# Optimization experiments

Hardware: AMD Instinct MI355X
Metric: run time of the kernel (lower is better)

Reference implementation:

```python
import jax, jax.numpy as jnp
import numpy as np

N_USERS = 50000
N_ENTITIES = 100000
N_FACTORS = 8
N_RELATIONS = 17  # weight has n_relations-1 = 16 rows
EMB = 64
N_EDGES = 2_000_000
NNZ = 2_000_000
SLOPE = 0.2


def setup_inputs() -> dict:
    key = jax.random.key(0)
    ks = jax.random.split(key, 16)
    inp = {
        "entity_emb": jax.random.normal(ks[0], (N_ENTITIES, EMB), jnp.float32),
        "user_emb": jax.random.normal(ks[1], (N_USERS, EMB), jnp.float32),
        "latent_emb": jax.random.normal(ks[2], (N_FACTORS, EMB), jnp.float32),
        "edge_index": jax.random.randint(ks[3], (2, N_EDGES), 0, N_ENTITIES, jnp.int32),
        "edge_type": jax.random.randint(ks[4], (N_EDGES,), 1, N_RELATIONS, jnp.int32),
        "interact_rows": jax.random.randint(ks[5], (NNZ,), 0, N_USERS, jnp.int32),
        "interact_cols": jax.random.randint(ks[6], (NNZ,), 0, N_ENTITIES, jnp.int32),
        "interact_vals": jax.random.uniform(ks[7], (NNZ,), jnp.float32),
        "weight": jax.random.normal(ks[8], (N_RELATIONS - 1, EMB), jnp.float32),
        "entity_cate_set": jax.random.randint(ks[9], (N_ENTITIES,), 1, 33, jnp.int32),
        # params (torch Linear convention: y = x @ W.T + b)
        "W_user_att": jax.random.normal(ks[10], (N_FACTORS, N_FACTORS), jnp.float32) * 0.1,
        "b_user_att": jnp.zeros((N_FACTORS,), jnp.float32),
        "W_weight_att": jax.random.normal(ks[11], (N_RELATIONS - 1, N_RELATIONS - 1), jnp.float32) * 0.1,
        "b_weight_att": jnp.zeros((N_RELATIONS - 1,), jnp.float32),
        "W1": jax.random.normal(ks[12], (EMB, EMB), jnp.float32) * 0.1,
        "b1": jnp.zeros((EMB,), jnp.float32),
        "W2": jax.random.normal(ks[13], (EMB, EMB), jnp.float32) * 0.1,
        "b2": jnp.zeros((EMB,), jnp.float32),
    }
    return inp


def _lin(x, W, b):
    return x @ W.T + b


def reference(entity_emb, user_emb, latent_emb, edge_index, edge_type,
              interact_rows, interact_cols, interact_vals, weight, entity_cate_set,
              W_user_att, b_user_att, W_weight_att, b_weight_att, W1, b1, W2, b2):
    head, tail = edge_index[0], edge_index[1]

    # KG aggregate: gather-multiply-scatter_mean (is_div=False branch)
    neigh = entity_emb[tail] * weight[edge_type - 1]            # [E, C]
    sums = jax.ops.segment_sum(neigh, head, num_segments=N_ENTITIES)
    cnt = jax.ops.segment_sum(jnp.ones((neigh.shape[0],), neigh.dtype),
                              head, num_segments=N_ENTITIES)
    entity_agg = sums / jnp.maximum(cnt, 1.0)[:, None]          # [N_ent, C]

    # user aggregate: sparse mm (COO) interact_mat @ entity_emb
    user_agg = jax.ops.segment_sum(interact_vals[:, None] * entity_emb[interact_cols],
                                   interact_rows, num_segments=N_USERS)  # [U, C]

    # user -> latent interest attention
    score_ = _lin(user_emb, W1, b1) @ _lin(latent_emb, W1, b1).T          # [U, F]
    score = jax.nn.softmax(jax.nn.leaky_relu(_lin(score_, W_user_att, b_user_att), SLOPE), axis=1)  # [U, F]

    score_rp = _lin(latent_emb, W2, b2) @ _lin(weight, W2, b2).T          # [F, R-1]
    latent_new = jax.nn.softmax(jax.nn.leaky_relu(_lin(score_rp, W_weight_att, b_weight_att), SLOPE), axis=-1) @ weight  # [F, C]

    # (disen_weight * score).sum(dim=1) == score @ latent_new
    user_agg = user_agg * (score @ latent_new) + user_agg
    return (entity_agg, user_agg, latent_new)
```

## Files before the change

### kernel.cpp

```cpp
#include <hip/hip_runtime.h>
#include <hip/hip_bf16.h>

#define N_USERS    50000
#define N_ENTITIES 100000
#define EMB        64
#define N_EDGES    2000000
#define NNZ        2000000
#define SLOPE      0.2f

#define KROWS   256
#define KSHIFT  8
#define NBK     391
#define UROWS   128
#define USHIFT  7
#define NBU     391
#define CAPK    8192
#define CAPU    7680
#define CHUNK   8192
#define PB      ((N_EDGES + CHUNK - 1) / CHUNK)

__global__ __launch_bounds__(512) void hist_both(const int* __restrict__ head,
                                                 const int* __restrict__ urows,
                                                 int* __restrict__ kgOffs,
                                                 int* __restrict__ uOffs) {
    __shared__ int lhk[NBK];
    __shared__ int lhu[NBU];
    int tid = threadIdx.x;
    for (int t = tid; t < NBK; t += 512) lhk[t] = 0;
    for (int t = tid; t < NBU; t += 512) lhu[t] = 0;
    __syncthreads();
    int base = blockIdx.x * CHUNK;
#pragma unroll 4
    for (int j = 0; j < CHUNK / 512; ++j) {
        int i = base + j * 512 + tid;
        if (i < N_EDGES) atomicAdd(&lhk[head[i] >> KSHIFT], 1);
        if (i < NNZ)     atomicAdd(&lhu[urows[i] >> USHIFT], 1);
    }
    __syncthreads();
    for (int t = tid; t < NBK; t += 512) { int c = lhk[t]; if (c) atomicAdd(&kgOffs[t], c); }
    for (int t = tid; t < NBU; t += 512) { int c = lhu[t]; if (c) atomicAdd(&uOffs[t], c); }
}

__global__ __launch_bounds__(512) void scan_both(int* __restrict__ kgOffs,
                                                 int* __restrict__ kgCur,
                                                 int* __restrict__ uOffs,
                                                 int* __restrict__ uCur) {
    __shared__ int tsum[512];
    int n     = (blockIdx.x == 0) ? NBK : NBU;
    int* offs = (blockIdx.x == 0) ? kgOffs : uOffs;
    int* cur  = (blockIdx.x == 0) ? kgCur  : uCur;
    int tid = threadIdx.x;
    int v = (tid < n) ? offs[tid] : 0;
    tsum[tid] = v;
    __syncthreads();
    for (int off = 1; off < 512; off <<= 1) {
        int t = (tid >= off) ? tsum[tid - off] : 0;
        __syncthreads();
        tsum[tid] += t;
        __syncthreads();
    }
    if (tid < n) { int e = tsum[tid] - v; offs[tid] = e; cur[tid] = e; }
    if (tid == n - 1) offs[n] = tsum[tid];
}

__global__ __launch_bounds__(512) void scatter_both(const int* __restrict__ head,
                                                    const int* __restrict__ tail,
                                                    const int* __restrict__ etype,
                                                    int* __restrict__ kgCur,
                                                    int* __restrict__ kgPay,
                                                    const int* __restrict__ urows,
                                                    const int* __restrict__ ucols,
                                                    const float* __restrict__ uvals,
                                                    int* __restrict__ uCur,
                                                    int2* __restrict__ uPay) {
    __shared__ int lh[NBK];
    __shared__ int lb[NBK];
    int tid = threadIdx.x;
    bool isKg = blockIdx.x < PB;
    int base = (isKg ? blockIdx.x : blockIdx.x - PB) * CHUNK;

    for (int t = tid; t < NBK; t += 512) lh[t] = 0;
    __syncthreads();
    if (isKg) {
#pragma unroll 4
        for (int j = 0; j < CHUNK / 512; ++j) {
            int i = base + j * 512 + tid;
            if (i < N_EDGES) atomicAdd(&lh[head[i] >> KSHIFT], 1);
        }
    } else {
#pragma unroll 4
        for (int j = 0; j < CHUNK / 512; ++j) {
            int i = base + j * 512 + tid;
            if (i < NNZ) atomicAdd(&lh[urows[i] >> USHIFT], 1);
        }
    }
    __syncthreads();
    int* cur = isKg ? kgCur : uCur;
    for (int t = tid; t < NBK; t += 512) {
        int c = lh[t];
        lb[t] = c ? atomicAdd(&cur[t], c) : 0;
        lh[t] = 0;
    }
    __syncthreads();
    if (isKg) {
#pragma unroll 4
        for (int j = 0; j < CHUNK / 512; ++j) {
            int i = base + j * 512 + tid;
            if (i < N_EDGES) {
                int h = head[i];
                int b = h >> KSHIFT;
                int p = lb[b] + atomicAdd(&lh[b], 1);
                kgPay[p] = tail[i] | ((etype[i] - 1) << 17) | ((h & (KROWS - 1)) << 21);
            }
        }
    } else {
#pragma unroll 4
        for (int j = 0; j < CHUNK / 512; ++j) {
            int i = base + j * 512 + tid;
            if (i < NNZ) {
                int r = urows[i];
                int b = r >> USHIFT;
                int p = lb[b] + atomicAdd(&lh[b], 1);
                uPay[p] = make_int2(ucols[i] | ((r & (UROWS - 1)) << 17),
                                    __float_as_int(uvals[i]));
            }
        }
    }
}

__global__ __launch_bounds__(1024, 8) void acc_both(
        const int* __restrict__ kgPay, const int* __restrict__ kgOffs,
        const int2* __restrict__ uPay, const int* __restrict__ uOffs,
        const float* __restrict__ entity_emb,
        const float* __restrict__ weight,
        const float* __restrict__ user_emb,
        const float* __restrict__ P,
        const float* __restrict__ cvec,
        const float* __restrict__ W_user_att,
        const float* __restrict__ b_user_att,
        const float* __restrict__ latent_new,
        float* __restrict__ ent_out,
        float* __restrict__ user_out) {
    __shared__ long long smem8[7873];
    int t = threadIdx.x, d = t & 63, wv = t >> 6;

    if (blockIdx.x < NBK) {
        int* spay = (int*)smem8;
        int* lcnt = spay + CAPK;
        int* lofs = lcnt + KROWS;
        int* sc   = lofs + KROWS + 1;
        int start = kgOffs[blockIdx.x], end = kgOffs[blockIdx.x + 1];
        int n = end - start; if (n > CAPK) n = CAPK;

        if (t < KROWS) lcnt[t] = 0;
        __syncthreads();
        for (int i = t; i < n; i += 1024)
            atomicAdd(&lcnt[(kgPay[start + i] >> 21) & (KROWS - 1)], 1);
        __syncthreads();
        if (t < KROWS) sc[t] = lcnt[t];
        __syncthreads();
        for (int off = 1; off < KROWS; off <<= 1) {
            int v = (t < KROWS && t >= off) ? sc[t - off] : 0;
            __syncthreads();
            if (t < KROWS) sc[t] += v;
            __syncthreads();
        }
        if (t < KROWS) { int e = sc[t] - lcnt[t]; lofs[t] = e; lcnt[t] = e; }
        if (t == 0) lofs[KROWS] = n;
        __syncthreads();
        for (int i = t; i < n; i += 1024) {
            int v = kgPay[start + i];
            int p = atomicAdd(&lcnt[(v >> 21) & (KROWS - 1)], 1);
            spay[p] = v;
        }
        __syncthreads();

        int rowbase = blockIdx.x * KROWS;
        for (int rr = 0; rr < KROWS / 16; ++rr) {
            int r = wv * (KROWS / 16) + rr;
            int gr = rowbase + r;
            if (gr >= N_ENTITIES) break;
            int s0 = lofs[r], e0 = lofs[r + 1];
            int cnt = e0 - s0;
            float acc = 0.f;
            int i = s0;
            for (; i + 7 < e0; i += 8) {
                float a0 = 0.f, a1 = 0.f;
#pragma unroll
                for (int u = 0; u < 8; u += 2) {
                    int va = spay[i + u], vb = spay[i + u + 1];
                    a0 += entity_emb[(va & 0x1FFFF) * EMB + d] * weight[((va >> 17) & 15) * EMB + d];
                    a1 += entity_emb[(vb & 0x1FFFF) * EMB + d] * weight[((vb >> 17) & 15) * EMB + d];
                }
                acc += a0 + a1;
            }
            for (; i < e0; ++i) {
                int v = spay[i];
                acc += entity_emb[(v & 0x1FFFF) * EMB + d] * weight[((v >> 17) & 15) * EMB + d];
            }
            for (int j = start + CAPK; j < end; ++j) {
                int v = kgPay[j];
                if (((v >> 21) & (KROWS - 1)) == r) {
                    acc += entity_emb[(v & 0x1FFFF) * EMB + d] * weight[((v >> 17) & 15) * EMB + d];
                    ++cnt;
                }
            }
            ent_out[gr * EMB + d] = acc / fmaxf((float)cnt, 1.f);
        }
    } else {
        int2* spay = (int2*)smem8;
        int* lcnt = (int*)(spay + CAPU);
        int* lofs = lcnt + UROWS;
        int* sc   = lofs + UROWS + 1;
        int bk = blockIdx.x - NBK;
        int start = uOffs[bk], end = uOffs[bk + 1];
        int n = end - start; if (n > CAPU) n = CAPU;

        if (t < UROWS) lcnt[t] = 0;
        __syncthreads();
        for (int i = t; i < n; i += 1024)
            atomicAdd(&lcnt[(uPay[start + i].x >> 17) & (UROWS - 1)], 1);
        __syncthreads();
        if (t < UROWS) sc[t] = lcnt[t];
        __syncthreads();
        for (int off = 1; off < UROWS; off <<= 1) {
            int v = (t < UROWS && t >= off) ? sc[t - off] : 0;
            __syncthreads();
            if (t < UROWS) sc[t] += v;
            __syncthreads();
        }
        if (t < UROWS) { int e = sc[t] - lcnt[t]; lofs[t] = e; lcnt[t] = e; }
        if (t == 0) lofs[UROWS] = n;
        __syncthreads();
        for (int i = t; i < n; i += 1024) {
            int2 v = uPay[start + i];
            int p = atomicAdd(&lcnt[(v.x >> 17) & (UROWS - 1)], 1);
            spay[p] = v;
        }
        __syncthreads();

        int rowbase = bk * UROWS;
        for (int rr = 0; rr < UROWS / 16; ++rr) {
            int r = wv * (UROWS / 16) + rr;
            int gr = rowbase + r;
            if (gr >= N_USERS) break;
            int s0 = lofs[r], e0 = lofs[r + 1];
            float acc = 0.f;
            int i = s0;
            for (; i + 7 < e0; i += 8) {
                float a0 = 0.f, a1 = 0.f;
#pragma unroll
                for (int u = 0; u < 8; u += 2) {
                    int2 va = spay[i + u], vb = spay[i + u + 1];
                    a0 += __int_as_float(va.y) * entity_emb[(va.x & 0x1FFFF) * EMB + d];
                    a1 += __int_as_float(vb.y) * entity_emb[(vb.x & 0x1FFFF) * EMB + d];
                }
                acc += a0 + a1;
            }
            for (; i < e0; ++i) {
                int2 v = spay[i];
                acc += __int_as_float(v.y) * entity_emb[(v.x & 0x1FFFF) * EMB + d];
            }
            for (int j = start + CAPU; j < end; ++j) {
                int2 v = uPay[j];
                if (((v.x >> 17) & (UROWS - 1)) == r)
                    acc += __int_as_float(v.y) * entity_emb[(v.x & 0x1FFFF) * EMB + d];
            }

            float ue = user_emb[gr * EMB + d];
            float s[8];
#pragma unroll
            for (int f = 0; f < 8; ++f) s[f] = ue * P[d * 8 + f];
#pragma unroll
            for (int off = 32; off; off >>= 1) {
#pragma unroll
                for (int f = 0; f < 8; ++f) s[f] += __shfl_xor(s[f], off, 64);
            }
#pragma unroll
            for (int f = 0; f < 8; ++f) s[f] += cvec[f];
            float att[8];
            float mx = -1e30f;
#pragma unroll
            for (int k = 0; k < 8; ++k) {
                float a = b_user_att[k];
#pragma unroll
                for (int j = 0; j < 8; ++j) a += s[j] * W_user_att[k * 8 + j];
                a = a > 0.f ? a : SLOPE * a;
                att[k] = a;
                mx = fmaxf(mx, a);
            }
            float sum = 0.f;
#pragma unroll
            for (int k = 0; k < 8; ++k) { att[k] = __expf(att[k] - mx); sum += att[k]; }
            float inv = 1.f / sum;
            float g = 0.f;
#pragma unroll
            for (int f = 0; f < 8; ++f) g += att[f] * inv * latent_new[f * EMB + d];
            user_out[gr * EMB + d] = acc * (1.f + g);
        }
    }
}

__global__ void small_dense(const float* __restrict__ latent_emb,
                            const float* __restrict__ weight,
                            const float* __restrict__ W_weight_att,
                            const float* __restrict__ b_weight_att,
                            const float* __restrict__ W1,
                            const float* __restrict__ b1,
                            const float* __restrict__ W2,
                            const float* __restrict__ b2,
                            float* __restrict__ P_out,
                            float* __restrict__ c_out,
                            float* __restrict__ latent_new_out) {
    __shared__ float lat1[8 * 64];
    __shared__ float lat2[8 * 64];
    __shared__ float wl2[16 * 64];
    __shared__ float srp[8 * 16];
    __shared__ float soft[8 * 16];
    int l = threadIdx.x;

    for (int f = 0; f < 8; ++f) {
        float a1 = b1[l], a2 = b2[l];
        for (int k = 0; k < 64; ++k) {
            float le = latent_emb[f * 64 + k];
            a1 += le * W1[l * 64 + k];
            a2 += le * W2[l * 64 + k];
        }
        lat1[f * 64 + l] = a1;
        lat2[f * 64 + l] = a2;
    }
    for (int r = 0; r < 16; ++r) {
        float a = b2[l];
        for (int k = 0; k < 64; ++k) a += weight[r * 64 + k] * W2[l * 64 + k];
        wl2[r * 64 + l] = a;
    }
    __syncthreads();

    for (int f = 0; f < 8; ++f) {
        float p = 0.f;
        for (int d = 0; d < 64; ++d) p += W1[d * 64 + l] * lat1[f * 64 + d];
        P_out[l * 8 + f] = p;
    }
    if (l < 8) {
        float cc = 0.f;
        for (int d = 0; d < 64; ++d) cc += b1[d] * lat1[l * 64 + d];
        c_out[l] = cc;
    }
    for (int idx = l; idx < 128; idx += 64) {
        int f = idx >> 4, r = idx & 15;
        float a = 0.f;
        for (int d = 0; d < 64; ++d) a += lat2[f * 64 + d] * wl2[r * 64 + d];
        srp[idx] = a;
    }
    __syncthreads();

    if (l < 8) {
        int f = l;
        float att[16];
        float mx = -1e30f;
        for (int k = 0; k < 16; ++k) {
            float a = b_weight_att[k];
            for (int j = 0; j < 16; ++j) a += srp[f * 16 + j] * W_weight_att[k * 16 + j];
            a = a > 0.f ? a : SLOPE * a;
            att[k] = a;
            mx = fmaxf(mx, a);
        }
        float s = 0.f;
        for (int k = 0; k < 16; ++k) { att[k] = expf(att[k] - mx); s += att[k]; }
        float inv = 1.f / s;
        for (int k = 0; k < 16; ++k) soft[f * 16 + k] = att[k] * inv;
    }
    __syncthreads();

    for (int f = 0; f < 8; ++f) {
        float a = 0.f;
        for (int r = 0; r < 16; ++r) a += soft[f * 16 + r] * weight[r * 64 + l];
        latent_new_out[f * 64 + l] = a;
    }
}

__global__ void kg_scatter(const int* __restrict__ head, const int* __restrict__ tail,
                           const int* __restrict__ etype,
                           const float* __restrict__ entity_emb,
                           const float* __restrict__ weight,
                           float* __restrict__ sums, float* __restrict__ cnt) {
    int gid = blockIdx.x * blockDim.x + threadIdx.x;
    int e = gid >> 6, d = threadIdx.x & 63;
    if (e >= N_EDGES) return;
    int h = head[e], t = tail[e], w = etype[e] - 1;
    float v = entity_emb[t * EMB + d] * weight[w * EMB + d];
    unsafeAtomicAdd(&sums[h * EMB + d], v);
    if (d == 0) unsafeAtomicAdd(&cnt[h], 1.0f);
}

__global__ void user_scatter(const int* __restrict__ rows, const int* __restrict__ cols,
                             const float* __restrict__ vals,
                             const float* __restrict__ entity_emb,
                             float* __restrict__ user_sums) {
    int gid = blockIdx.x * blockDim.x + threadIdx.x;
    int e = gid >> 6, d = threadIdx.x & 63;
    if (e >= NNZ) return;
    float v = vals[e] * entity_emb[cols[e] * EMB + d];
    unsafeAtomicAdd(&user_sums[rows[e] * EMB + d], v);
}

__global__ void entity_div(float* __restrict__ ent, const float* __restrict__ cnt) {
    int gid = blockIdx.x * blockDim.x + threadIdx.x;
    if (gid >= N_ENTITIES * EMB) return;
    float c = cnt[gid >> 6];
    ent[gid] = ent[gid] / fmaxf(c, 1.0f);
}

__global__ void user_finalize(const float* __restrict__ user_emb,
                              const float* __restrict__ P,
                              const float* __restrict__ c,
                              const float* __restrict__ W_user_att,
                              const float* __restrict__ b_user_att,
                              const float* __restrict__ latent_new,
                              float* __restrict__ user_out) {
    int gid = blockIdx.x * blockDim.x + threadIdx.x;
    int u = gid >> 6, lane = threadIdx.x & 63;
    if (u >= N_USERS) return;
    float ue = user_emb[u * 64 + lane];
    float s[8];
#pragma unroll
    for (int f = 0; f < 8; ++f) s[f] = ue * P[lane * 8 + f];
#pragma unroll
    for (int off = 32; off; off >>= 1)
#pragma unroll
        for (int f = 0; f < 8; ++f) s[f] += __shfl_xor(s[f], off, 64);
#pragma unroll
    for (int f = 0; f < 8; ++f) s[f] += c[f];
    float att[8], mx = -1e30f;
#pragma unroll
    for (int k = 0; k < 8; ++k) {
        float a = b_user_att[k];
#pragma unroll
        for (int j = 0; j < 8; ++j) a += s[j] * W_user_att[k * 8 + j];
        a = a > 0.f ? a : SLOPE * a;
        att[k] = a;
        mx = fmaxf(mx, a);
    }
    float sum = 0.f;
#pragma unroll
    for (int k = 0; k < 8; ++k) { att[k] = expf(att[k] - mx); sum += att[k]; }
    float inv = 1.f / sum, g = 0.f;
#pragma unroll
    for (int f = 0; f < 8; ++f) g += att[f] * inv * latent_new[f * 64 + lane];
    float ua = user_out[u * 64 + lane];
    user_out[u * 64 + lane] = ua * (1.f + g);
}

extern "C" void kernel_launch(void* const* d_in, const int* in_sizes, int n_in,
                              void* d_out, int out_size, void* d_ws, size_t ws_size,
                              hipStream_t stream) {
    const float* entity_emb   = (const float*)d_in[0];
    const float* user_emb     = (const float*)d_in[1];
    const float* latent_emb   = (const float*)d_in[2];
    const int*   edge_index   = (const int*)d_in[3];
    const int*   edge_type    = (const int*)d_in[4];
    const int*   irows        = (const int*)d_in[5];
    const int*   icols        = (const int*)d_in[6];
    const float* ivals        = (const float*)d_in[7];
    const float* weight       = (const float*)d_in[8];
    const float* W_user_att   = (const float*)d_in[10];
    const float* b_user_att   = (const float*)d_in[11];
    const float* W_weight_att = (const float*)d_in[12];
    const float* b_weight_att = (const float*)d_in[13];
    const float* W1           = (const float*)d_in[14];
    const float* b1           = (const float*)d_in[15];
    const float* W2           = (const float*)d_in[16];
    const float* b2           = (const float*)d_in[17];

    float* out      = (float*)d_out;
    float* ent_out  = out;
    float* user_out = out + (size_t)N_ENTITIES * EMB;
    float* lat_out  = user_out + (size_t)N_USERS * EMB;

    const int* head = edge_index;
    const int* tail = edge_index + N_EDGES;

    int* ws_i = (int*)d_ws;
    int*   kgOffs = ws_i;
    int*   uOffs  = kgOffs + (NBK + 1);
    int*   kgCur  = uOffs + (NBU + 1);
    int*   uCur   = kgCur + NBK;
    int*   kgPay  = uCur + NBU;
    int2*  uPay   = (int2*)(kgPay + N_EDGES);
    float* Pbuf   = (float*)(uPay + NNZ);
    float* cbuf   = Pbuf + 64 * 8;
    size_t need_bytes = (size_t)((NBK + 1) + (NBU + 1) + NBK + NBU +
                                 N_EDGES + 2 * (size_t)NNZ + 512 + 8) * 4;

    if (ws_size >= need_bytes) {
        hipMemsetAsync(kgOffs, 0, (size_t)((NBK + 1) + (NBU + 1)) * sizeof(int), stream);

        hist_both<<<PB, 512, 0, stream>>>(head, irows, kgOffs, uOffs);
        scan_both<<<2, 512, 0, stream>>>(kgOffs, kgCur, uOffs, uCur);
        scatter_both<<<2 * PB, 512, 0, stream>>>(head, tail, edge_type, kgCur, kgPay,
                                                 irows, icols, ivals, uCur, uPay);
        small_dense<<<1, 64, 0, stream>>>(latent_emb, weight, W_weight_att,
                                          b_weight_att, W1, b1, W2, b2,
                                          Pbuf, cbuf, lat_out);
        acc_both<<<NBK + NBU, 1024, 0, stream>>>(kgPay, kgOffs, uPay, uOffs,
                                                 entity_emb, weight, user_emb,
                                                 Pbuf, cbuf, W_user_att, b_user_att,
                                                 lat_out, ent_out, user_out);
    } else {
        float* cnt   = (float*)d_ws;
        float* Pbuf2 = cnt + N_ENTITIES;
        float* cbuf2 = Pbuf2 + 64 * 8;
        hipMemsetAsync(ent_out, 0,
                       (size_t)(N_ENTITIES + N_USERS) * EMB * sizeof(float), stream);
        hipMemsetAsync(cnt, 0, N_ENTITIES * sizeof(float), stream);
        int blocks_edges = (N_EDGES * 64) / 256;
        kg_scatter<<<blocks_edges, 256, 0, stream>>>(head, tail, edge_type, entity_emb,
                                                     weight, ent_out, cnt);
        user_scatter<<<blocks_edges, 256, 0, stream>>>(irows, icols, ivals, entity_emb,
                                                       user_out);
        small_dense<<<1, 64, 0, stream>>>(latent_emb, weight, W_weight_att,
                                          b_weight_att, W1, b1, W2, b2,
                                          Pbuf2, cbuf2, lat_out);
        user_finalize<<<(N_USERS * 64) / 256, 256, 0, stream>>>(user_emb, Pbuf2, cbuf2,
                                                                W_user_att, b_user_att,
                                                                lat_out, user_out);
        entity_div<<<(N_ENTITIES * EMB) / 256, 256, 0, stream>>>(ent_out, cnt);
    }
}
```

Before: 442.4 us.

## Use persistent work-queue blocks for accumulation and fold small_dense into scatter

The accumulation kernel now launches a fixed 512 persistent blocks that pull bucket indices from a global atomic counter, taking user buckets first and then KG buckets, instead of one block per bucket. The small dense attention computation moves into an extra block of the scatter kernel, which removes a separate launch. The scatter kernel also keeps the head/row indices it loaded for the histogram in registers and reuses them in the placement pass rather than reloading them. These changes aim to cut launch overhead, tail imbalance and redundant global loads, at the cost of a serialising atomic per work item and higher register pressure in scatter.

```diff
diff --git a/kernel.cpp b/kernel.cpp
--- a/kernel.cpp
+++ b/kernel.cpp
@@ -1,5 +1,4 @@
 #include <hip/hip_runtime.h>
-#include <hip/hip_bf16.h>
 
 #define N_USERS    50000
 #define N_ENTITIES 100000
@@ -17,7 +16,10 @@
 #define CAPK    8192
 #define CAPU    7680
 #define CHUNK   8192
+#define EPT     (CHUNK / 512)
 #define PB      ((N_EDGES + CHUNK - 1) / CHUNK)
+#define NQ      (NBK + NBU)
+#define ACCBLK  512
 
 __global__ __launch_bounds__(512) void hist_both(const int* __restrict__ head,
                                                  const int* __restrict__ urows,
@@ -31,7 +33,7 @@
     __syncthreads();
     int base = blockIdx.x * CHUNK;
 #pragma unroll 4
-    for (int j = 0; j < CHUNK / 512; ++j) {
+    for (int j = 0; j < EPT; ++j) {
         int i = base + j * 512 + tid;
         if (i < N_EDGES) atomicAdd(&lhk[head[i] >> KSHIFT], 1);
         if (i < NNZ)     atomicAdd(&lhu[urows[i] >> USHIFT], 1);
@@ -63,6 +65,105 @@
     if (tid == n - 1) offs[n] = tsum[tid];
 }
 
+__device__ void small_dense_body(int l,
+                                 const float* __restrict__ latent_emb,
+                                 const float* __restrict__ weight,
+                                 const float* __restrict__ W_weight_att,
+                                 const float* __restrict__ b_weight_att,
+                                 const float* __restrict__ W1,
+                                 const float* __restrict__ b1,
+                                 const float* __restrict__ W2,
+                                 const float* __restrict__ b2,
+                                 float* __restrict__ P_out,
+                                 float* __restrict__ c_out,
+                                 float* __restrict__ latent_new_out) {
+    __shared__ float lat1[8 * 64];
+    __shared__ float lat2[8 * 64];
+    __shared__ float wl2[16 * 64];
+    __shared__ float srp[8 * 16];
+    __shared__ float soft[8 * 16];
+
+    if (l < 64) {
+        for (int f = 0; f < 8; ++f) {
+            float a1 = b1[l], a2 = b2[l];
+            for (int k = 0; k < 64; ++k) {
+                float le = latent_emb[f * 64 + k];
+                a1 += le * W1[l * 64 + k];
+                a2 += le * W2[l * 64 + k];
+            }
+            lat1[f * 64 + l] = a1;
+            lat2[f * 64 + l] = a2;
+        }
+        for (int r = 0; r < 16; ++r) {
+            float a = b2[l];
+            for (int k = 0; k < 64; ++k) a += weight[r * 64 + k] * W2[l * 64 + k];
+            wl2[r * 64 + l] = a;
+        }
+    }
+    __syncthreads();
+
+    if (l < 64) {
+        for (int f = 0; f < 8; ++f) {
+            float p = 0.f;
+            for (int d = 0; d < 64; ++d) p += W1[d * 64 + l] * lat1[f * 64 + d];
+            P_out[l * 8 + f] = p;
+        }
+        if (l < 8) {
+            float cc = 0.f;
+            for (int d = 0; d < 64; ++d) cc += b1[d] * lat1[l * 64 + d];
+            c_out[l] = cc;
+        }
+        for (int idx = l; idx < 128; idx += 64) {
+            int f = idx >> 4, r = idx & 15;
+            float a = 0.f;
+            for (int d = 0; d < 64; ++d) a += lat2[f * 64 + d] * wl2[r * 64 + d];
+            srp[idx] = a;
+        }
+    }
+    __syncthreads();
+
+    if (l < 8) {
+        int f = l;
+        float att[16];
+        float mx = -1e30f;
+        for (int k = 0; k < 16; ++k) {
+            float a = b_weight_att[k];
+            for (int j = 0; j < 16; ++j) a += srp[f * 16 + j] * W_weight_att[k * 16 + j];
+            a = a > 0.f ? a : SLOPE * a;
+            att[k] = a;
+            mx = fmaxf(mx, a);
+        }
+        float s = 0.f;
+        for (int k = 0; k < 16; ++k) { att[k] = expf(att[k] - mx); s += att[k]; }
+        float inv = 1.f / s;
+        for (int k = 0; k < 16; ++k) soft[f * 16 + k] = att[k] * inv;
+    }
+    __syncthreads();
+
+    if (l < 64) {
+        for (int f = 0; f < 8; ++f) {
+            float a = 0.f;
+            for (int r = 0; r < 16; ++r) a += soft[f * 16 + r] * weight[r * 64 + l];
+            latent_new_out[f * 64 + l] = a;
+        }
+    }
+}
+
+__global__ void small_dense(const float* __restrict__ latent_emb,
+                            const float* __restrict__ weight,
+                            const float* __restrict__ W_weight_att,
+                            const float* __restrict__ b_weight_att,
+                            const float* __restrict__ W1,
+                            const float* __restrict__ b1,
+                            const float* __restrict__ W2,
+                            const float* __restrict__ b2,
+                            float* __restrict__ P_out,
+                            float* __restrict__ c_out,
+                            float* __restrict__ latent_new_out) {
+    small_dense_body(threadIdx.x, latent_emb, weight, W_weight_att, b_weight_att,
+                     W1, b1, W2, b2, P_out, c_out, latent_new_out);
+}
+
 __global__ __launch_bounds__(512) void scatter_both(const int* __restrict__ head,
                                                     const int* __restrict__ tail,
                                                     const int* __restrict__ etype,
@@ -72,30 +173,46 @@
                                                     const int* __restrict__ ucols,
                                                     const float* __restrict__ uvals,
                                                     int* __restrict__ uCur,
-                                                    int2* __restrict__ uPay) {
+                                                    int2* __restrict__ uPay,
+                                                    const float* __restrict__ latent_emb,
+                                                    const float* __restrict__ weight,
+                                                    const float* __restrict__ W_weight_att,
+                                                    const float* __restrict__ b_weight_att,
+                                                    const float* __restrict__ W1,
+                                                    const float* __restrict__ b1,
+                                                    const float* __restrict__ W2,
+                                                    const float* __restrict__ b2,
+                                                    float* __restrict__ Pbuf,
+                                                    float* __restrict__ cbuf,
+                                                    float* __restrict__ lat_out) {
+    if (blockIdx.x == 2 * PB) {
+        small_dense_body(threadIdx.x, latent_emb, weight, W_weight_att,
+                         b_weight_att, W1, b1, W2, b2, Pbuf, cbuf, lat_out);
+        return;
+    }
+
     __shared__ int lh[NBK];
     __shared__ int lb[NBK];
     int tid = threadIdx.x;
     bool isKg = blockIdx.x < PB;
     int base = (isKg ? blockIdx.x : blockIdx.x - PB) * CHUNK;
+    int nTot = isKg ? N_EDGES : NNZ;
+    int shift = isKg ? KSHIFT : USHIFT;
+    const int* src = isKg ? head : urows;
+    int* cur = isKg ? kgCur : uCur;
 
     for (int t = tid; t < NBK; t += 512) lh[t] = 0;
     __syncthreads();
-    if (isKg) {
-#pragma unroll 4
-        for (int j = 0; j < CHUNK / 512; ++j) {
-            int i = base + j * 512 + tid;
-            if (i < N_EDGES) atomicAdd(&lh[head[i] >> KSHIFT], 1);
-        }
-    } else {
-#pragma unroll 4
-        for (int j = 0; j < CHUNK / 512; ++j) {
-            int i = base + j * 512 + tid;
-            if (i < NNZ) atomicAdd(&lh[urows[i] >> USHIFT], 1);
-        }
-    }
-    __syncthreads();
-    int* cur = isKg ? kgCur : uCur;
+
+    int hreg[EPT];
+#pragma unroll
+    for (int j = 0; j < EPT; ++j) {
+        int i = base + j * 512 + tid;
+        int h = (i < nTot) ? src[i] : -1;
+        hreg[j] = h;
+        if (h >= 0) atomicAdd(&lh[h >> shift], 1);
+    }
+    __syncthreads();
     for (int t = tid; t < NBK; t += 512) {
         int c = lh[t];
         lb[t] = c ? atomicAdd(&cur[t], c) : 0;
@@ -103,25 +220,25 @@
     }
     __syncthreads();
     if (isKg) {
-#pragma unroll 4
-        for (int j = 0; j < CHUNK / 512; ++j) {
-            int i = base + j * 512 + tid;
-            if (i < N_EDGES) {
-                int h = head[i];
+#pragma unroll
+        for (int j = 0; j < EPT; ++j) {
+            int h = hreg[j];
+            if (h >= 0) {
+                int i = base + j * 512 + tid;
                 int b = h >> KSHIFT;
                 int p = lb[b] + atomicAdd(&lh[b], 1);
                 kgPay[p] = tail[i] | ((etype[i] - 1) << 17) | ((h & (KROWS - 1)) << 21);
             }
         }
     } else {
-#pragma unroll 4
-        for (int j = 0; j < CHUNK / 512; ++j) {
-            int i = base + j * 512 + tid;
-            if (i < NNZ) {
-                int r = urows[i];
-                int b = r >> USHIFT;
+#pragma unroll
+        for (int j = 0; j < EPT; ++j) {
+            int h = hreg[j];
+            if (h >= 0) {
+                int i = base + j * 512 + tid;
+                int b = h >> USHIFT;
                 int p = lb[b] + atomicAdd(&lh[b], 1);
-                uPay[p] = make_int2(ucols[i] | ((r & (UROWS - 1)) << 17),
+                uPay[p] = make_int2(ucols[i] | ((h & (UROWS - 1)) << 17),
                                     __float_as_int(uvals[i]));
             }
         }
@@ -139,243 +256,176 @@
         const float* __restrict__ W_user_att,
         const float* __restrict__ b_user_att,
         const float* __restrict__ latent_new,
+        int* __restrict__ qCtr,
         float* __restrict__ ent_out,
         float* __restrict__ user_out) {
     __shared__ long long smem8[7873];
+    __shared__ int sbk;
     int t = threadIdx.x, d = t & 63, wv = t >> 6;
 
-    if (blockIdx.x < NBK) {
-        int* spay = (int*)smem8;
-        int* lcnt = spay + CAPK;
-        int* lofs = lcnt + KROWS;
-        int* sc   = lofs + KROWS + 1;
-        int start = kgOffs[blockIdx.x], end = kgOffs[blockIdx.x + 1];
-        int n = end - start; if (n > CAPK) n = CAPK;
-
-        if (t < KROWS) lcnt[t] = 0;
+    for (;;) {
         __syncthreads();
-        for (int i = t; i < n; i += 1024)
-            atomicAdd(&lcnt[(kgPay[start + i] >> 21) & (KROWS - 1)], 1);
+        if (t == 0) sbk = atomicAdd(qCtr, 1);
         __syncthreads();
-        if (t < KROWS) sc[t] = lcnt[t];
-        __syncthreads();
-        for (int off = 1; off < KROWS; off <<= 1) {
-            int v = (t < KROWS && t >= off) ? sc[t - off] : 0;
-            __syncthreads();
-            if (t < KROWS) sc[t] += v;
-            __syncthreads();
-        }
-        if (t < KROWS) { int e = sc[t] - lcnt[t]; lofs[t] = e; lcnt[t] = e; }
-        if (t == 0) lofs[KROWS] = n;
-        __syncthreads();
-        for (int i = t; i < n; i += 1024) {
-            int v = kgPay[start + i];
-            int p = atomicAdd(&lcnt[(v >> 21) & (KROWS - 1)], 1);
-            spay[p] = v;
-        }
-        __syncthreads();
-
-        int rowbase = blockIdx.x * KROWS;
-        for (int rr = 0; rr < KROWS / 16; ++rr) {
-            int r = wv * (KROWS / 16) + rr;
-            int gr = rowbase + r;
-            if (gr >= N_ENTITIES) break;
-            int s0 = lofs[r], e0 = lofs[r + 1];
-            int cnt = e0 - s0;
-            float acc = 0.f;
-            int i = s0;
-            for (; i + 7 < e0; i += 8) {
-                float a0 = 0.f, a1 = 0.f;
-#pragma unroll
-                for (int u = 0; u < 8; u += 2) {
-                    int va = spay[i + u], vb = spay[i + u + 1];
-                    a0 += entity_emb[(va & 0x1FFFF) * EMB + d] * weight[((va >> 17) & 15) * EMB + d];
-                    a1 += entity_emb[(vb & 0x1FFFF) * EMB + d] * weight[((vb >> 17) & 15) * EMB + d];
-                }
-                acc += a0 + a1;
-            }
-            for (; i < e0; ++i) {
-                int v = spay[i];
-                acc += entity_emb[(v & 0x1FFFF) * EMB + d] * weight[((v >> 17) & 15) * EMB + d];
-            }
-            for (int j = start + CAPK; j < end; ++j) {
-                int v = kgPay[j];
-                if (((v >> 21) & (KROWS - 1)) == r) {
+        int q = sbk;
+        if (q >= NQ) return;
+
+        if (q < NBU) {
+            int2* spay = (int2*)smem8;
+            int* lcnt = (int*)(spay + CAPU);
+            int* lofs = lcnt + UROWS;
+            int* sc   = lofs + UROWS + 1;
+            int bk = q;
+            int start = uOffs[bk], end = uOffs[bk + 1];
+            int n = end - start; if (n > CAPU) n = CAPU;
+
+            if (t < UROWS) lcnt[t] = 0;
+            __syncthreads();
+            for (int i = t; i < n; i += 1024)
+                atomicAdd(&lcnt[(uPay[start + i].x >> 17) & (UROWS - 1)], 1);
+            __syncthreads();
+            if (t < UROWS) sc[t] = lcnt[t];
+            __syncthreads();
+            for (int off = 1; off < UROWS; off <<= 1) {
+                int v = (t < UROWS && t >= off) ? sc[t - off] : 0;
+                __syncthreads();
+                if (t < UROWS) sc[t] += v;
+                __syncthreads();
+            }
+            if (t < UROWS) { int e = sc[t] - lcnt[t]; lofs[t] = e; lcnt[t] = e; }
+            if (t == 0) lofs[UROWS] = n;
+            __syncthreads();
+            for (int i = t; i < n; i += 1024) {
+                int2 v = uPay[start + i];
+                int p = atomicAdd(&lcnt[(v.x >> 17) & (UROWS - 1)], 1);
+                spay[p] = v;
+            }
+            __syncthreads();
+
+            int rowbase = bk * UROWS;
+            for (int rr = 0; rr < UROWS / 16; ++rr) {
+                int r = wv * (UROWS / 16) + rr;
+                int gr = rowbase + r;
+                if (gr >= N_USERS) break;
+                int s0 = lofs[r], e0 = lofs[r + 1];
+                float acc = 0.f;
+                int i = s0;
+                for (; i + 7 < e0; i += 8) {
+                    float a0 = 0.f, a1 = 0.f;
+#pragma unroll
+                    for (int u = 0; u < 8; u += 2) {
+                        int2 va = spay[i + u], vb = spay[i + u + 1];
+                        a0 += __int_as_float(va.y) * entity_emb[(va.x & 0x1FFFF) * EMB + d];
+                        a1 += __int_as_float(vb.y) * entity_emb[(vb.x & 0x1FFFF) * EMB + d];
+                    }
+                    acc += a0 + a1;
+                }
+                for (; i < e0; ++i) {
+                    int2 v = spay[i];
+                    acc += __int_as_float(v.y) * entity_emb[(v.x & 0x1FFFF) * EMB + d];
+                }
+                for (int j = start + CAPU; j < end; ++j) {
+                    int2 v = uPay[j];
+                    if (((v.x >> 17) & (UROWS - 1)) == r)
+                        acc += __int_as_float(v.y) * entity_emb[(v.x & 0x1FFFF) * EMB + d];
+                }
+
+                float ue = user_emb[gr * EMB + d];
+                float s[8];
+#pragma unroll
+                for (int f = 0; f < 8; ++f) s[f] = ue * P[d * 8 + f];
+#pragma unroll
+                for (int off = 32; off; off >>= 1) {
+#pragma unroll
+                    for (int f = 0; f < 8; ++f) s[f] += __shfl_xor(s[f], off, 64);
+                }
+#pragma unroll
+                for (int f = 0; f < 8; ++f) s[f] += cvec[f];
+                float att[8];
+                float mx = -1e30f;
+#pragma unroll
+                for (int k = 0; k < 8; ++k) {
+                    float a = b_user_att[k];
+#pragma unroll
+                    for (int j = 0; j < 8; ++j) a += s[j] * W_user_att[k * 8 + j];
+                    a = a > 0.f ? a : SLOPE * a;
+                    att[k] = a;
+                    mx = fmaxf(mx, a);
+                }
+                float sum = 0.f;
+#pragma unroll
+                for (int k = 0; k < 8; ++k) { att[k] = __expf(att[k] - mx); sum += att[k]; }
+                float inv = 1.f / sum;
+                float g = 0.f;
+#pragma unroll
+                for (int f = 0; f < 8; ++f) g += att[f] * inv * latent_new[f * EMB + d];
+                user_out[gr * EMB + d] = acc * (1.f + g);
+            }
+        } else {
+            int* spay = (int*)smem8;
+            int* lcnt = spay + CAPK;
+            int* lofs = lcnt + KROWS;
+            int* sc   = lofs + KROWS + 1;
+            int bk = q - NBU;
+            int start = kgOffs[bk], end = kgOffs[bk + 1];
+            int n = end - start; if (n > CAPK) n = CAPK;
+
+            if (t < KROWS) lcnt[t] = 0;
+            __syncthreads();
+            for (int i = t; i < n; i += 1024)
+                atomicAdd(&lcnt[(kgPay[start + i] >> 21) & (KROWS - 1)], 1);
+            __syncthreads();
+            if (t < KROWS) sc[t] = lcnt[t];
+            __syncthreads();
+            for (int off = 1; off < KROWS; off <<= 1) {
+                int v = (t < KROWS && t >= off) ? sc[t - off] : 0;
+                __syncthreads();
+                if (t < KROWS) sc[t] += v;
+                __syncthreads();
+            }
+            if (t < KROWS) { int e = sc[t] - lcnt[t]; lofs[t] = e; lcnt[t] = e; }
+            if (t == 0) lofs[KROWS] = n;
+            __syncthreads();
+            for (int i = t; i < n; i += 1024) {
+                int v = kgPay[start + i];
+                int p = atomicAdd(&lcnt[(v >> 21) & (KROWS - 1)], 1);
+                spay[p] = v;
+            }
+            __syncthreads();
+
+            int rowbase = bk * KROWS;
+            for (int rr = 0; rr < KROWS / 16; ++rr) {
+                int r = wv * (KROWS / 16) + rr;
+                int gr = rowbase + r;
+                if (gr >= N_ENTITIES) break;
+                int s0 = lofs[r], e0 = lofs[r + 1];
+                int cnt = e0 - s0;
+                float acc = 0.f;
+                int i = s0;
+                for (; i + 7 < e0; i += 8) {
+                    float a0 = 0.f, a1 = 0.f;
+#pragma unroll
+                    for (int u = 0; u < 8; u += 2) {
+                        int va = spay[i + u], vb = spay[i + u + 1];
+                        a0 += entity_emb[(va & 0x1FFFF) * EMB + d] * weight[((va >> 17) & 15) * EMB + d];
+                        a1 += entity_emb[(vb & 0x1FFFF) * EMB + d] * weight[((vb >> 17) & 15) * EMB + d];
+                    }
+                    acc += a0 + a1;
+                }
+                for (; i < e0; ++i) {
+                    int v = spay[i];
                     acc += entity_emb[(v & 0x1FFFF) * EMB + d] * weight[((v >> 17) & 15) * EMB + d];
-                    ++cnt;
-                }
-            }
-            ent_out[gr * EMB + d] = acc / fmaxf((float)cnt, 1.f);
-        }
-    } else {
-        int2* spay = (int2*)smem8;
-        int* lcnt = (int*)(spay + CAPU);
-        int* lofs = lcnt + UROWS;
-        int* sc   = lofs + UROWS + 1;
-        int bk = blockIdx.x - NBK;
-        int start = uOffs[bk], end = uOffs[bk + 1];
-        int n = end - start; if (n > CAPU) n = CAPU;
-
-        if (t < UROWS) lcnt[t] = 0;
-        __syncthreads();
-        for (int i = t; i < n; i += 1024)
-            atomicAdd(&lcnt[(uPay[start + i].x >> 17) & (UROWS - 1)], 1);
-        __syncthreads();
-        if (t < UROWS) sc[t] = lcnt[t];
-        __syncthreads();
-        for (int off = 1; off < UROWS; off <<= 1) {
-            int v = (t < UROWS && t >= off) ? sc[t - off] : 0;
-            __syncthreads();
-            if (t < UROWS) sc[t] += v;
-            __syncthreads();
-        }
-        if (t < UROWS) { int e = sc[t] - lcnt[t]; lofs[t] = e; lcnt[t] = e; }
-        if (t == 0) lofs[UROWS] = n;
-        __syncthreads();
-        for (int i = t; i < n; i += 1024) {
-            int2 v = uPay[start + i];
-            int p = atomicAdd(&lcnt[(v.x >> 17) & (UROWS - 1)], 1);
-            spay[p] = v;
-        }
-        __syncthreads();
-
-        int rowbase = bk * UROWS;
-        for (int rr = 0; rr < UROWS / 16; ++rr) {
-            int r = wv * (UROWS / 16) + rr;
-            int gr = rowbase + r;
-            if (gr >= N_USERS) break;
-            int s0 = lofs[r], e0 = lofs[r + 1];
-            float acc = 0.f;
-            int i = s0;
-            for (; i + 7 < e0; i += 8) {
-                float a0 = 0.f, a1 = 0.f;
-#pragma unroll
-                for (int u = 0; u < 8; u += 2) {
-                    int2 va = spay[i + u], vb = spay[i + u + 1];
-                    a0 += __int_as_float(va.y) * entity_emb[(va.x & 0x1FFFF) * EMB + d];
-                    a1 += __int_as_float(vb.y) * entity_emb[(vb.x & 0x1FFFF) * EMB + d];
-                }
-                acc += a0 + a1;
-            }
-            for (; i < e0; ++i) {
-                int2 v = spay[i];
-                acc += __int_as_float(v.y) * entity_emb[(v.x & 0x1FFFF) * EMB + d];
-            }
-            for (int j = start + CAPU; j < end; ++j) {
-                int2 v = uPay[j];
-                if (((v.x >> 17) & (UROWS - 1)) == r)
-                    acc += __int_as_float(v.y) * entity_emb[(v.x & 0x1FFFF) * EMB + d];
-            }
-
-            float ue = user_emb[gr * EMB + d];
-            float s[8];
-#pragma unroll
-            for (int f = 0; f < 8; ++f) s[f] = ue * P[d * 8 + f];
-#pragma unroll
-            for (int off = 32; off; off >>= 1) {
-#pragma unroll
-                for (int f = 0; f < 8; ++f) s[f] += __shfl_xor(s[f], off, 64);
-            }
-#pragma unroll
-            for (int f = 0; f < 8; ++f) s[f] += cvec[f];
-            float att[8];
-            float mx = -1e30f;
-#pragma unroll
-            for (int k = 0; k < 8; ++k) {
-                float a = b_user_att[k];
-#pragma unroll
-                for (int j = 0; j < 8; ++j) a += s[j] * W_user_att[k * 8 + j];
-                a = a > 0.f ? a : SLOPE * a;
-                att[k] = a;
-                mx = fmaxf(mx, a);
-            }
-            float sum = 0.f;
-#pragma unroll
-            for (int k = 0; k < 8; ++k) { att[k] = __expf(att[k] - mx); sum += att[k]; }
-            float inv = 1.f / sum;
-            float g = 0.f;
-#pragma unroll
-            for (int f = 0; f < 8; ++f) g += att[f] * inv * latent_new[f * EMB + d];
-            user_out[gr * EMB + d] = acc * (1.f + g);
-        }
-    }
-}
-
-__global__ void small_dense(const float* __restrict__ latent_emb,
-                            const float* __restrict__ weight,
-                            const float* __restrict__ W_weight_att,
-                            const float* __restrict__ b_weight_att,
-                            const float* __restrict__ W1,
-                            const float* __restrict__ b1,
-                            const float* __restrict__ W2,
-                            const float* __restrict__ b2,
-                            float* __restrict__ P_out,
-                            float* __restrict__ c_out,
-                            float* __restrict__ latent_new_out) {
-    __shared__ float lat1[8 * 64];
-    __shared__ float lat2[8 * 64];
-    __shared__ float wl2[16 * 64];
-    __shared__ float srp[8 * 16];
-    __shared__ float soft[8 * 16];
-    int l = threadIdx.x;
-
-    for (int f = 0; f < 8; ++f) {
-        float a1 = b1[l], a2 = b2[l];
-        for (int k = 0; k < 64; ++k) {
-            float le = latent_emb[f * 64 + k];
-            a1 += le * W1[l * 64 + k];
-            a2 += le * W2[l * 64 + k];
-        }
-        lat1[f * 64 + l] = a1;
-        lat2[f * 64 + l] = a2;
-    }
-    for (int r = 0; r < 16; ++r) {
-        float a = b2[l];
-        for (int k = 0; k < 64; ++k) a += weight[r * 64 + k] * W2[l * 64 + k];
-        wl2[r * 64 + l] = a;
-    }
-    __syncthreads();
-
-    for (int f = 0; f < 8; ++f) {
-        float p = 0.f;
-        for (int d = 0; d < 64; ++d) p += W1[d * 64 + l] * lat1[f * 64 + d];
-        P_out[l * 8 + f] = p;
-    }
-    if (l < 8) {
-        float cc = 0.f;
-        for (int d = 0; d < 64; ++d) cc += b1[d] * lat1[l * 64 + d];
-        c_out[l] = cc;
-    }
-    for (int idx = l; idx < 128; idx += 64) {
-        int f = idx >> 4, r = idx & 15;
-        float a = 0.f;
-        for (int d = 0; d < 64; ++d) a += lat2[f * 64 + d] * wl2[r * 64 + d];
-        srp[idx] = a;
-    }
-    __syncthreads();
-
-    if (l < 8) {
-        int f = l;
-        float att[16];
-        float mx = -1e30f;
-        for (int k = 0; k < 16; ++k) {
-            float a = b_weight_att[k];
-            for (int j = 0; j < 16; ++j) a += srp[f * 16 + j] * W_weight_att[k * 16 + j];
-            a = a > 0.f ? a : SLOPE * a;
-            att[k] = a;
-            mx = fmaxf(mx, a);
-        }
-        float s = 0.f;
-        for (int k = 0; k < 16; ++k) { att[k] = expf(att[k] - mx); s += att[k]; }
-        float inv = 1.f / s;
-        for (int k = 0; k < 16; ++k) soft[f * 16 + k] = att[k] * inv;
-    }
-    __syncthreads();
-
-    for (int f = 0; f < 8; ++f) {
-        float a = 0.f;
-        for (int r = 0; r < 16; ++r) a += soft[f * 16 + r] * weight[r * 64 + l];
-        latent_new_out[f * 64 + l] = a;
+                }
+                for (int j = start + CAPK; j < end; ++j) {
+                    int v = kgPay[j];
+                    if (((v >> 21) & (KROWS - 1)) == r) {
+                        acc += entity_emb[(v & 0x1FFFF) * EMB + d] * weight[((v >> 17) & 15) * EMB + d];
+                        ++cnt;
+                    }
+                }
+                ent_out[gr * EMB + d] = acc / fmaxf((float)cnt, 1.f);
+            }
+        }
     }
 }
 
@@ -483,29 +533,31 @@
     int* ws_i = (int*)d_ws;
     int*   kgOffs = ws_i;
     int*   uOffs  = kgOffs + (NBK + 1);
-    int*   kgCur  = uOffs + (NBU + 1);
+    int*   qCtr   = uOffs + (NBU + 1);
+    int*   kgCur  = qCtr + 2;
     int*   uCur   = kgCur + NBK;
     int*   kgPay  = uCur + NBU;
     int2*  uPay   = (int2*)(kgPay + N_EDGES);
     float* Pbuf   = (float*)(uPay + NNZ);
     float* cbuf   = Pbuf + 64 * 8;
-    size_t need_bytes = (size_t)((NBK + 1) + (NBU + 1) + NBK + NBU +
+    size_t need_bytes = (size_t)((NBK + 1) + (NBU + 1) + 2 + NBK + NBU +
                                  N_EDGES + 2 * (size_t)NNZ + 512 + 8) * 4;
 
     if (ws_size >= need_bytes) {
-        hipMemsetAsync(kgOffs, 0, (size_t)((NBK + 1) + (NBU + 1)) * sizeof(int), stream);
+        hipMemsetAsync(kgOffs, 0,
+                       (size_t)((NBK + 1) + (NBU + 1) + 2) * sizeof(int), stream);
 
         hist_both<<<PB, 512, 0, stream>>>(head, irows, kgOffs, uOffs);
         scan_both<<<2, 512, 0, stream>>>(kgOffs, kgCur, uOffs, uCur);
-        scatter_both<<<2 * PB, 512, 0, stream>>>(head, tail, edge_type, kgCur, kgPay,
-                                                 irows, icols, ivals, uCur, uPay);
-        small_dense<<<1, 64, 0, stream>>>(latent_emb, weight, W_weight_att,
-                                          b_weight_att, W1, b1, W2, b2,
-                                          Pbuf, cbuf, lat_out);
-        acc_both<<<NBK + NBU, 1024, 0, stream>>>(kgPay, kgOffs, uPay, uOffs,
-                                                 entity_emb, weight, user_emb,
-                                                 Pbuf, cbuf, W_user_att, b_user_att,
-                                                 lat_out, ent_out, user_out);
+        scatter_both<<<2 * PB + 1, 512, 0, stream>>>(head, tail, edge_type, kgCur, kgPay,
+                                                     irows, icols, ivals, uCur, uPay,
+                                                     latent_emb, weight, W_weight_att,
+                                                     b_weight_att, W1, b1, W2, b2,
+                                                     Pbuf, cbuf, lat_out);
+        acc_both<<<ACCBLK, 1024, 0, stream>>>(kgPay, kgOffs, uPay, uOffs,
+                                              entity_emb, weight, user_emb,
+                                              Pbuf, cbuf, W_user_att, b_user_att,
+                                              lat_out, qCtr, ent_out, user_out);
     } else {
         float* cnt   = (float*)d_ws;
         float* Pbuf2 = cnt + N_ENTITIES;
```

Measured after the change: 397.7 us. 10.1% less time.
